# Kernel optimization log

Hardware: AMD Instinct MI355X
Metric: run time of the kernel (lower is better)

Reference implementation:

```python
import jax, jax.numpy as jnp
import numpy as np

B, N, F, H, L = 8, 512, 32, 64, 2

def setup_inputs() -> dict:
    key = jax.random.key(0)
    ks = jax.random.split(key, 16)
    s = lambda fan_in: 1.0 / np.sqrt(fan_in)
    return {
        "x": jax.random.normal(ks[0], (B, N, F), dtype=jnp.float32),
        # node encoder: Linear(F, H), stored as [in, out]
        "W_enc": jax.random.uniform(ks[1], (F, H), minval=-s(F), maxval=s(F)),
        "b_enc": jax.random.uniform(ks[2], (H,), minval=-s(F), maxval=s(F)),
        # edge MLP: Linear(2H, H) then Linear(H, 1)
        "W_e1": jax.random.uniform(ks[3], (2 * H, H), minval=-s(2 * H), maxval=s(2 * H)),
        "b_e1": jax.random.uniform(ks[4], (H,), minval=-s(2 * H), maxval=s(2 * H)),
        "W_e2": jax.random.uniform(ks[5], (H,), minval=-s(H), maxval=s(H)),
        "b_e2": jax.random.uniform(ks[6], (), minval=-s(H), maxval=s(H)),
        # per-layer message Linear(H, H)
        "W_msg": jax.random.uniform(ks[7], (L, H, H), minval=-s(H), maxval=s(H)),
        "b_msg": jax.random.uniform(ks[8], (L, H), minval=-s(H), maxval=s(H)),
        # per-layer GRUCell(H, H): gates ordered [r, z, n], stored as [in, 3H]
        "W_ih": jax.random.uniform(ks[9], (L, H, 3 * H), minval=-s(H), maxval=s(H)),
        "b_ih": jax.random.uniform(ks[10], (L, 3 * H), minval=-s(H), maxval=s(H)),
        "W_hh": jax.random.uniform(ks[11], (L, H, 3 * H), minval=-s(H), maxval=s(H)),
        "b_hh": jax.random.uniform(ks[12], (L, 3 * H), minval=-s(H), maxval=s(H)),
        # output Linear(H, 1)
        "W_out": jax.random.uniform(ks[13], (H, 1), minval=-s(H), maxval=s(H)),
        "b_out": jax.random.uniform(ks[14], (1,), minval=-s(H), maxval=s(H)),
    }

def reference(x, W_enc, b_enc, W_e1, b_e1, W_e2, b_e2, W_msg, b_msg,
              W_ih, b_ih, W_hh, b_hh, W_out, b_out):
    # Node encoding (dropout is eval-mode identity)
    h = jax.nn.relu(x @ W_enc + b_enc)  # [B, N, H]

    # Edge MLP on pairwise concat [h_i, h_j]: split W_e1 so we never build the 2H concat
    Wa, Wb = W_e1[:H], W_e1[H:]
    zi = h @ Wa                           # contribution of h_i, [B, N, H]
    zj = h @ Wb                           # contribution of h_j, [B, N, H]
    e = jax.nn.relu(zi[:, :, None, :] + zj[:, None, :, :] + b_e1)  # [B, N, N, H]
    logits = jnp.einsum('bijh,h->bij', e, W_e2) + b_e2             # [B, N, N]

    eye = jnp.eye(logits.shape[-1], dtype=bool)
    logits = jnp.where(eye[None], -jnp.inf, logits)
    adj = jax.nn.softmax(logits, axis=-1)
    adj = jnp.nan_to_num(adj, nan=0.0, posinf=0.0, neginf=0.0)

    for l in range(L):
        m = jnp.einsum('bij,bjh->bih', adj, h)             # message aggregation
        m = jax.nn.relu(m @ W_msg[l] + b_msg[l])
        # GRUCell update (gates [r, z, n])
        gi = m @ W_ih[l] + b_ih[l]
        gh = h @ W_hh[l] + b_hh[l]
        ir, iz, inn = jnp.split(gi, 3, axis=-1)
        hr, hz, hn = jnp.split(gh, 3, axis=-1)
        r = jax.nn.sigmoid(ir + hr)
        z = jax.nn.sigmoid(iz + hz)
        n = jnp.tanh(inn + r * hn)
        h = (1.0 - z) * n + z * h

    graph_emb = jnp.mean(h, axis=1)       # [B, H]
    return graph_emb @ W_out + b_out      # [B, 1]
```

## Files before the change

### kernel.cpp

```cpp
#include <hip/hip_runtime.h>
#include <math.h>

#define BB 8
#define NN 512
#define FF 32
#define HH 64
#define NEG_BIG (-1.0e30f)

__device__ __forceinline__ float lane_bcast(float v, int l) {
    return __int_as_float(__builtin_amdgcn_readlane(__float_as_int(v), l));
}

__global__ __launch_bounds__(256) void encode_kernel(
    const float* __restrict__ x, const float* __restrict__ W_enc,
    const float* __restrict__ b_enc, const float* __restrict__ W_e1,
    const float* __restrict__ b_e1,
    float* __restrict__ h, float* __restrict__ zi, float* __restrict__ zj)
{
    const int t = threadIdx.x;
    const int hh = t & 63;
    const int qu = __builtin_amdgcn_readfirstlane(t >> 6);
    const int gR = blockIdx.x * 4 + qu;

    const float xv = x[gR * FF + (hh & 31)];
    float acc = b_enc[hh];
#pragma unroll 8
    for (int k = 0; k < FF; ++k)
        acc = fmaf(lane_bcast(xv, k), W_enc[k * HH + hh], acc);
    const float hval = fmaxf(acc, 0.f);
    h[gR * HH + hh] = hval;

    float z1 = b_e1[hh], z2 = 0.f;
#pragma unroll 8
    for (int k = 0; k < HH; ++k) {
        const float hk = lane_bcast(hval, k);
        z1 = fmaf(hk, W_e1[k * HH + hh], z1);
        z2 = fmaf(hk, W_e1[(HH + k) * HH + hh], z2);
    }
    zi[gR * HH + hh] = z1;
    zj[gR * HH + hh] = z2;
}

template <int MODE>
__global__ __launch_bounds__(256, 2) void adjlayer_kernel(
    const float* __restrict__ zi, const float* __restrict__ zj,
    const float* __restrict__ We2, const float* __restrict__ be2,
    float* __restrict__ adjw, const float* __restrict__ h_in,
    const float* __restrict__ Wmsg, const float* __restrict__ bmsg,
    const float* __restrict__ Wih, const float* __restrict__ bih,
    const float* __restrict__ Whh, const float* __restrict__ bhh,
    float* __restrict__ h_out, float* __restrict__ partial)
{
    const int b  = blockIdx.x >> 6;
    const int i0 = (blockIdx.x & 63) << 3;
    const int t  = threadIdx.x;
    const int tj = t & 63;
    const int w  = __builtin_amdgcn_readfirstlane(t >> 6);
    const int gR0 = b * NN + i0;

    __shared__ float smem[NN * 17];
    __shared__ float mml[8][66];
    __shared__ float hol[8][66];
    __shared__ float redm[4][8];
    __shared__ float reds[4][8];

    float (*zjs)[17] = (float (*)[17])smem;
#define RED(p, r, c)       smem[(((p) * 8) + (r)) * 66 + (c)]
#define GP(h2, k2, r, g, c) smem[((((((h2) * 2 + (k2)) * 8) + (r)) * 3 + (g)) * 66) + (c)]

    const int r0 = 2 * w, r1 = 2 * w + 1;
    hol[r0][tj] = h_in[(size_t)(gR0 + r0) * HH + tj];
    hol[r1][tj] = h_in[(size_t)(gR0 + r1) * HH + tj];

    float va[8][2];
    if (MODE == 0) {
        float zir[8];
#pragma unroll
        for (int r = 0; r < 8; ++r) zir[r] = zi[(size_t)(gR0 + r) * HH + tj];
        const float wv = We2[tj];
        const float bias2 = be2[0];
        float acc[8][2];
#pragma unroll
        for (int r = 0; r < 8; ++r) { acc[r][0] = bias2; acc[r][1] = bias2; }

        for (int kp = 0; kp < 4; ++kp) {
            __syncthreads();
#pragma unroll
            for (int u = 0; u < 8; ++u) {
                const int i4 = t + u * 256;
                const int row = i4 >> 2, c4 = i4 & 3;
                *(float4*)&zjs[row][c4 * 4] =
                    ((const float4*)(zj + (size_t)(b * NN + row) * HH))[kp * 4 + c4];
            }
            __syncthreads();
            const int j0 = 128 * w + tj, j1 = j0 + 64;
#pragma unroll
            for (int kk = 0; kk < 16; ++kk) {
                const int k = (kp << 4) + kk;
                const float wk = lane_bcast(wv, k);
                const float zj0 = zjs[j0][kk];
                const float zj1 = zjs[j1][kk];
#pragma unroll
                for (int r = 0; r < 8; ++r) {
                    const float zv = lane_bcast(zir[r], k);
                    acc[r][0] = fmaf(fmaxf(zv + zj0, 0.f), wk, acc[r][0]);
                    acc[r][1] = fmaf(fmaxf(zv + zj1, 0.f), wk, acc[r][1]);
                }
            }
        }
#pragma unroll
        for (int r = 0; r < 8; ++r)
#pragma unroll
            for (int c = 0; c < 2; ++c)
                if (128 * w + 64 * c + tj == i0 + r) acc[r][c] = NEG_BIG;

#pragma unroll
        for (int r = 0; r < 8; ++r) {
            float m = fmaxf(acc[r][0], acc[r][1]);
#pragma unroll
            for (int off = 32; off >= 1; off >>= 1) m = fmaxf(m, __shfl_xor(m, off));
            if (tj == 0) redm[w][r] = m;
        }
        __syncthreads();
        float M[8];
#pragma unroll
        for (int r = 0; r < 8; ++r)
            M[r] = fmaxf(fmaxf(redm[0][r], redm[1][r]),
                         fmaxf(redm[2][r], redm[3][r]));
#pragma unroll
        for (int r = 0; r < 8; ++r) {
            const float e0 = __expf(acc[r][0] - M[r]);
            const float e1 = __expf(acc[r][1] - M[r]);
            va[r][0] = e0; va[r][1] = e1;
            float s = e0 + e1;
#pragma unroll
            for (int off = 32; off >= 1; off >>= 1) s += __shfl_xor(s, off);
            if (tj == 0) reds[w][r] = s;
        }
        __syncthreads();
#pragma unroll
        for (int r = 0; r < 8; ++r) {
            const float inv = 1.0f /
                (reds[0][r] + reds[1][r] + reds[2][r] + reds[3][r]);
            va[r][0] *= inv; va[r][1] *= inv;
            adjw[(size_t)(gR0 + r) * NN + 128 * w + tj]      = va[r][0];
            adjw[(size_t)(gR0 + r) * NN + 128 * w + 64 + tj] = va[r][1];
        }
    } else {
#pragma unroll
        for (int r = 0; r < 8; ++r) {
            va[r][0] = adjw[(size_t)(gR0 + r) * NN + 128 * w + tj];
            va[r][1] = adjw[(size_t)(gR0 + r) * NN + 128 * w + 64 + tj];
        }
    }

    {
        const float* hq = h_in + ((size_t)b * NN + 128 * w) * HH + tj;
        float mac[8] = {0.f, 0.f, 0.f, 0.f, 0.f, 0.f, 0.f, 0.f};
#pragma unroll
        for (int c = 0; c < 2; ++c) {
#pragma unroll 4
            for (int jj = 0; jj < 64; jj += 4) {
                const float h0 = hq[(64 * c + jj + 0) * HH];
                const float h1 = hq[(64 * c + jj + 1) * HH];
                const float h2 = hq[(64 * c + jj + 2) * HH];
                const float h3 = hq[(64 * c + jj + 3) * HH];
#pragma unroll
                for (int r = 0; r < 8; ++r) {
                    float a = fmaf(lane_bcast(va[r][c], jj + 0), h0, mac[r]);
                    a = fmaf(lane_bcast(va[r][c], jj + 1), h1, a);
                    a = fmaf(lane_bcast(va[r][c], jj + 2), h2, a);
                    mac[r] = fmaf(lane_bcast(va[r][c], jj + 3), h3, a);
                }
            }
        }
        if (MODE == 0) __syncthreads();
#pragma unroll
        for (int r = 0; r < 8; ++r) RED(w, r, tj) = mac[r];
    }
    __syncthreads();

    float mm0, mm1;
    {
        const float m0 = RED(0, r0, tj) + RED(1, r0, tj) + RED(2, r0, tj) + RED(3, r0, tj);
        const float m1 = RED(0, r1, tj) + RED(1, r1, tj) + RED(2, r1, tj) + RED(3, r1, tj);
        mm0 = bmsg[tj]; mm1 = mm0;
#pragma unroll 8
        for (int k = 0; k < HH; ++k) {
            const float wm = Wmsg[k * HH + tj];
            mm0 = fmaf(lane_bcast(m0, k), wm, mm0);
            mm1 = fmaf(lane_bcast(m1, k), wm, mm1);
        }
        mm0 = fmaxf(mm0, 0.f); mm1 = fmaxf(mm1, 0.f);
        mml[r0][tj] = mm0; mml[r1][tj] = mm1;
    }
    __syncthreads();

    {
        const int half = w >> 1, kh = w & 1;
        const float* Wg = half ? Whh : Wih;
        const float* bg = half ? bhh : bih;
        float sreg[8];
#pragma unroll
        for (int r = 0; r < 8; ++r) sreg[r] = half ? hol[r][tj] : mml[r][tj];
        float g0[8], g1[8], g2[8];
#pragma unroll
        for (int r = 0; r < 8; ++r) {
            g0[r] = kh ? 0.f : bg[tj];
            g1[r] = kh ? 0.f : bg[64 + tj];
            g2[r] = kh ? 0.f : bg[128 + tj];
        }
        const int k0 = kh * 32;
#pragma unroll 4
        for (int kk = 0; kk < 32; ++kk) {
            const float* wk = Wg + (size_t)(k0 + kk) * 192;
            const float w0 = wk[tj], w1 = wk[64 + tj], w2 = wk[128 + tj];
#pragma unroll
            for (int r = 0; r < 8; ++r) {
                const float s = lane_bcast(sreg[r], k0 + kk);
                g0[r] = fmaf(s, w0, g0[r]);
                g1[r] = fmaf(s, w1, g1[r]);
                g2[r] = fmaf(s, w2, g2[r]);
            }
        }
#pragma unroll
        for (int r = 0; r < 8; ++r) {
            GP(half, kh, r, 0, tj) = g0[r];
            GP(half, kh, r, 1, tj) = g1[r];
            GP(half, kh, r, 2, tj) = g2[r];
        }
    }
    __syncthreads();

    float hs0 = 0.f, hs1 = 0.f;
#pragma unroll
    for (int p = 0; p < 2; ++p) {
        const int rr = p ? r1 : r0;
        const float ir  = GP(0, 0, rr, 0, tj) + GP(0, 1, rr, 0, tj);
        const float iz  = GP(0, 0, rr, 1, tj) + GP(0, 1, rr, 1, tj);
        const float inn = GP(0, 0, rr, 2, tj) + GP(0, 1, rr, 2, tj);
        const float hr  = GP(1, 0, rr, 0, tj) + GP(1, 1, rr, 0, tj);
        const float hz  = GP(1, 0, rr, 1, tj) + GP(1, 1, rr, 1, tj);
        const float hn  = GP(1, 0, rr, 2, tj) + GP(1, 1, rr, 2, tj);
        const float rg = 1.f / (1.f + __expf(-(ir + hr)));
        const float zg = 1.f / (1.f + __expf(-(iz + hz)));
        const float ng = tanhf(inn + rg * hn);
        const float hnew = (1.f - zg) * ng + zg * hol[rr][tj];
        h_out[(size_t)(gR0 + rr) * HH + tj] = hnew;
        if (p) hs1 = hnew; else hs0 = hnew;
    }

    if (MODE == 1) {
        __syncthreads();
        mml[r0][tj] = hs0; mml[r1][tj] = hs1;
        __syncthreads();
        if (w == 0) {
            float s = 0.f;
#pragma unroll
            for (int r = 0; r < 8; ++r) s += mml[r][tj];
            partial[blockIdx.x * 64 + tj] = s;
        }
    }
#undef RED
#undef GP
}

__global__ __launch_bounds__(64) void readout_kernel(
    const float* __restrict__ partial, const float* __restrict__ W_out,
    const float* __restrict__ b_out, float* __restrict__ out)
{
    const int b = blockIdx.x;
    const int hh = threadIdx.x;
    float s = 0.f;
#pragma unroll 8
    for (int c = 0; c < 64; ++c)
        s += partial[(b * 64 + c) * 64 + hh];
    float v = s * (1.0f / NN) * W_out[hh];
#pragma unroll
    for (int off = 32; off >= 1; off >>= 1) v += __shfl_xor(v, off);
    if (hh == 0) out[b] = v + b_out[0];
}

extern "C" void kernel_launch(void* const* d_in, const int* in_sizes, int n_in,
                              void* d_out, int out_size, void* d_ws, size_t ws_size,
                              hipStream_t stream)
{
    const float* x     = (const float*)d_in[0];
    const float* W_enc = (const float*)d_in[1];
    const float* b_enc = (const float*)d_in[2];
    const float* W_e1  = (const float*)d_in[3];
    const float* b_e1  = (const float*)d_in[4];
    const float* W_e2  = (const float*)d_in[5];
    const float* b_e2  = (const float*)d_in[6];
    const float* W_msg = (const float*)d_in[7];
    const float* b_msg = (const float*)d_in[8];
    const float* W_ih  = (const float*)d_in[9];
    const float* b_ih  = (const float*)d_in[10];
    const float* W_hh  = (const float*)d_in[11];
    const float* b_hh  = (const float*)d_in[12];
    const float* W_out = (const float*)d_in[13];
    const float* b_out = (const float*)d_in[14];
    float* out = (float*)d_out;

    float* ws  = (float*)d_ws;
    float* h0  = ws;
    float* h1  = h0 + BB * NN * HH;
    float* zi  = h1 + BB * NN * HH;
    float* zj  = zi + BB * NN * HH;
    float* prt = zj + BB * NN * HH;
    float* adjw = prt + 512 * 64;

    encode_kernel<<<BB * NN / 4, 256, 0, stream>>>(x, W_enc, b_enc, W_e1, b_e1, h0, zi, zj);

    adjlayer_kernel<0><<<BB * (NN / 8), 256, 0, stream>>>(
        zi, zj, W_e2, b_e2, adjw, h0,
        W_msg, b_msg, W_ih, b_ih, W_hh, b_hh, h1, nullptr);
    adjlayer_kernel<1><<<BB * (NN / 8), 256, 0, stream>>>(
        zi, zj, W_e2, b_e2, adjw, h1,
        W_msg + HH * HH, b_msg + HH,
        W_ih + HH * 3 * HH, b_ih + 3 * HH, W_hh + HH * 3 * HH, b_hh + 3 * HH,
        h0, prt);

    readout_kernel<<<BB, 64, 0, stream>>>(prt, W_out, b_out, out);
}
```

Before: 82.92 us.

## Transpose zj in global memory and widen adjacency/layer kernel to 512 threads

The encoder now writes zj in a transposed [B, H, N] layout. Each thread of the adjacency kernel can then read its column j directly and coalesced from global memory, with no staging through shared memory. The kernel moves from 256 to 512 threads, so each thread handles one j column instead of two and the shared zj staging buffer is dropped. The softmax, message and GRU stages are re-split across 8 waves to match. The zi values and We2 weights are now read as uniform global loads instead of lane broadcasts. This trades shared-memory traffic and barriers for more global/scalar loads, with higher occupancy limits set via launch bounds.

```diff
diff --git a/kernel.cpp b/kernel.cpp
--- a/kernel.cpp
+++ b/kernel.cpp
@@ -15,7 +15,7 @@
     const float* __restrict__ x, const float* __restrict__ W_enc,
     const float* __restrict__ b_enc, const float* __restrict__ W_e1,
     const float* __restrict__ b_e1,
-    float* __restrict__ h, float* __restrict__ zi, float* __restrict__ zj)
+    float* __restrict__ h, float* __restrict__ zi, float* __restrict__ zjT)
 {
     const int t = threadIdx.x;
     const int hh = t & 63;
@@ -38,12 +38,12 @@
         z2 = fmaf(hk, W_e1[(HH + k) * HH + hh], z2);
     }
     zi[gR * HH + hh] = z1;
-    zj[gR * HH + hh] = z2;
+    zjT[((size_t)(gR >> 9) * HH + hh) * NN + (gR & (NN - 1))] = z2;
 }
 
 template <int MODE>
-__global__ __launch_bounds__(256, 2) void adjlayer_kernel(
-    const float* __restrict__ zi, const float* __restrict__ zj,
+__global__ __launch_bounds__(512, 4) void adjlayer_kernel(
+    const float* __restrict__ zi, const float* __restrict__ zjT,
     const float* __restrict__ We2, const float* __restrict__ be2,
     float* __restrict__ adjw, const float* __restrict__ h_in,
     const float* __restrict__ Wmsg, const float* __restrict__ bmsg,
@@ -57,66 +57,50 @@
     const int tj = t & 63;
     const int w  = __builtin_amdgcn_readfirstlane(t >> 6);
     const int gR0 = b * NN + i0;
-
-    __shared__ float smem[NN * 17];
+    const int j   = 64 * w + tj;
+
+    __shared__ float smem[6336];
     __shared__ float mml[8][66];
     __shared__ float hol[8][66];
-    __shared__ float redm[4][8];
-    __shared__ float reds[4][8];
-
-    float (*zjs)[17] = (float (*)[17])smem;
-#define RED(p, r, c)       smem[(((p) * 8) + (r)) * 66 + (c)]
-#define GP(h2, k2, r, g, c) smem[((((((h2) * 2 + (k2)) * 8) + (r)) * 3 + (g)) * 66) + (c)]
-
-    const int r0 = 2 * w, r1 = 2 * w + 1;
-    hol[r0][tj] = h_in[(size_t)(gR0 + r0) * HH + tj];
-    hol[r1][tj] = h_in[(size_t)(gR0 + r1) * HH + tj];
-
-    float va[8][2];
+    __shared__ float redm[8][8];
+    __shared__ float reds[8][8];
+#define RED(p, r, c)        smem[(((p) * 8) + (r)) * 66 + (c)]
+#define GP(h2, k2, r, g, c) smem[(((((h2) * 2 + (k2)) * 8 + (r)) * 3 + (g)) * 66) + (c)]
+
+    hol[w][tj] = h_in[(size_t)(gR0 + w) * HH + tj];
+
+    float va[8];
     if (MODE == 0) {
-        float zir[8];
-#pragma unroll
-        for (int r = 0; r < 8; ++r) zir[r] = zi[(size_t)(gR0 + r) * HH + tj];
-        const float wv = We2[tj];
+        const float* zib = zi + (size_t)gR0 * HH;
+        const float* ztb = zjT + (size_t)b * HH * NN + j;
         const float bias2 = be2[0];
-        float acc[8][2];
-#pragma unroll
-        for (int r = 0; r < 8; ++r) { acc[r][0] = bias2; acc[r][1] = bias2; }
-
-        for (int kp = 0; kp < 4; ++kp) {
-            __syncthreads();
-#pragma unroll
-            for (int u = 0; u < 8; ++u) {
-                const int i4 = t + u * 256;
-                const int row = i4 >> 2, c4 = i4 & 3;
-                *(float4*)&zjs[row][c4 * 4] =
-                    ((const float4*)(zj + (size_t)(b * NN + row) * HH))[kp * 4 + c4];
-            }
-            __syncthreads();
-            const int j0 = 128 * w + tj, j1 = j0 + 64;
-#pragma unroll
-            for (int kk = 0; kk < 16; ++kk) {
-                const int k = (kp << 4) + kk;
-                const float wk = lane_bcast(wv, k);
-                const float zj0 = zjs[j0][kk];
-                const float zj1 = zjs[j1][kk];
+        float acc[8];
+#pragma unroll
+        for (int r = 0; r < 8; ++r) acc[r] = bias2;
+
+        for (int kc = 0; kc < 8; ++kc) {
+            float zt[8];
+#pragma unroll
+            for (int kk = 0; kk < 8; ++kk)
+                zt[kk] = ztb[(size_t)(kc * 8 + kk) * NN];
+#pragma unroll
+            for (int kk = 0; kk < 8; ++kk) {
+                const int k = kc * 8 + kk;
+                const float wk = We2[k];
 #pragma unroll
                 for (int r = 0; r < 8; ++r) {
-                    const float zv = lane_bcast(zir[r], k);
-                    acc[r][0] = fmaf(fmaxf(zv + zj0, 0.f), wk, acc[r][0]);
-                    acc[r][1] = fmaf(fmaxf(zv + zj1, 0.f), wk, acc[r][1]);
+                    const float zv = zib[r * HH + k];
+                    acc[r] = fmaf(fmaxf(zv + zt[kk], 0.f), wk, acc[r]);
                 }
             }
         }
 #pragma unroll
         for (int r = 0; r < 8; ++r)
-#pragma unroll
-            for (int c = 0; c < 2; ++c)
-                if (128 * w + 64 * c + tj == i0 + r) acc[r][c] = NEG_BIG;
-
-#pragma unroll
-        for (int r = 0; r < 8; ++r) {
-            float m = fmaxf(acc[r][0], acc[r][1]);
+            if (j == i0 + r) acc[r] = NEG_BIG;
+
+#pragma unroll
+        for (int r = 0; r < 8; ++r) {
+            float m = acc[r];
 #pragma unroll
             for (int off = 32; off >= 1; off >>= 1) m = fmaxf(m, __shfl_xor(m, off));
             if (tj == 0) redm[w][r] = m;
@@ -124,15 +108,17 @@
         __syncthreads();
         float M[8];
 #pragma unroll
-        for (int r = 0; r < 8; ++r)
-            M[r] = fmaxf(fmaxf(redm[0][r], redm[1][r]),
-                         fmaxf(redm[2][r], redm[3][r]));
-#pragma unroll
-        for (int r = 0; r < 8; ++r) {
-            const float e0 = __expf(acc[r][0] - M[r]);
-            const float e1 = __expf(acc[r][1] - M[r]);
-            va[r][0] = e0; va[r][1] = e1;
-            float s = e0 + e1;
+        for (int r = 0; r < 8; ++r) {
+            float m = redm[0][r];
+#pragma unroll
+            for (int p = 1; p < 8; ++p) m = fmaxf(m, redm[p][r]);
+            M[r] = m;
+        }
+#pragma unroll
+        for (int r = 0; r < 8; ++r) {
+            const float e = __expf(acc[r] - M[r]);
+            va[r] = e;
+            float s = e;
 #pragma unroll
             for (int off = 32; off >= 1; off >>= 1) s += __shfl_xor(s, off);
             if (tj == 0) reds[w][r] = s;
@@ -140,72 +126,56 @@
         __syncthreads();
 #pragma unroll
         for (int r = 0; r < 8; ++r) {
-            const float inv = 1.0f /
-                (reds[0][r] + reds[1][r] + reds[2][r] + reds[3][r]);
-            va[r][0] *= inv; va[r][1] *= inv;
-            adjw[(size_t)(gR0 + r) * NN + 128 * w + tj]      = va[r][0];
-            adjw[(size_t)(gR0 + r) * NN + 128 * w + 64 + tj] = va[r][1];
+            float s = reds[0][r];
+#pragma unroll
+            for (int p = 1; p < 8; ++p) s += reds[p][r];
+            va[r] *= 1.0f / s;
+            adjw[(size_t)(gR0 + r) * NN + j] = va[r];
         }
     } else {
 #pragma unroll
-        for (int r = 0; r < 8; ++r) {
-            va[r][0] = adjw[(size_t)(gR0 + r) * NN + 128 * w + tj];
-            va[r][1] = adjw[(size_t)(gR0 + r) * NN + 128 * w + 64 + tj];
-        }
-    }
-
-    {
-        const float* hq = h_in + ((size_t)b * NN + 128 * w) * HH + tj;
+        for (int r = 0; r < 8; ++r)
+            va[r] = adjw[(size_t)(gR0 + r) * NN + j];
+    }
+
+    {
+        const float* hq = h_in + ((size_t)b * NN + 64 * w) * HH + tj;
         float mac[8] = {0.f, 0.f, 0.f, 0.f, 0.f, 0.f, 0.f, 0.f};
-#pragma unroll
-        for (int c = 0; c < 2; ++c) {
 #pragma unroll 4
-            for (int jj = 0; jj < 64; jj += 4) {
-                const float h0 = hq[(64 * c + jj + 0) * HH];
-                const float h1 = hq[(64 * c + jj + 1) * HH];
-                const float h2 = hq[(64 * c + jj + 2) * HH];
-                const float h3 = hq[(64 * c + jj + 3) * HH];
-#pragma unroll
-                for (int r = 0; r < 8; ++r) {
-                    float a = fmaf(lane_bcast(va[r][c], jj + 0), h0, mac[r]);
-                    a = fmaf(lane_bcast(va[r][c], jj + 1), h1, a);
-                    a = fmaf(lane_bcast(va[r][c], jj + 2), h2, a);
-                    mac[r] = fmaf(lane_bcast(va[r][c], jj + 3), h3, a);
-                }
-            }
-        }
-        if (MODE == 0) __syncthreads();
+        for (int jj = 0; jj < 64; ++jj) {
+            const float hv = hq[(size_t)jj * HH];
+#pragma unroll
+            for (int r = 0; r < 8; ++r)
+                mac[r] = fmaf(lane_bcast(va[r], jj), hv, mac[r]);
+        }
 #pragma unroll
         for (int r = 0; r < 8; ++r) RED(w, r, tj) = mac[r];
     }
     __syncthreads();
 
-    float mm0, mm1;
-    {
-        const float m0 = RED(0, r0, tj) + RED(1, r0, tj) + RED(2, r0, tj) + RED(3, r0, tj);
-        const float m1 = RED(0, r1, tj) + RED(1, r1, tj) + RED(2, r1, tj) + RED(3, r1, tj);
-        mm0 = bmsg[tj]; mm1 = mm0;
-#pragma unroll 8
-        for (int k = 0; k < HH; ++k) {
-            const float wm = Wmsg[k * HH + tj];
-            mm0 = fmaf(lane_bcast(m0, k), wm, mm0);
-            mm1 = fmaf(lane_bcast(m1, k), wm, mm1);
-        }
-        mm0 = fmaxf(mm0, 0.f); mm1 = fmaxf(mm1, 0.f);
-        mml[r0][tj] = mm0; mml[r1][tj] = mm1;
+    {
+        float m = RED(0, w, tj);
+#pragma unroll
+        for (int p = 1; p < 8; ++p) m += RED(p, w, tj);
+        float mmv = bmsg[tj];
+#pragma unroll 8
+        for (int k = 0; k < HH; ++k)
+            mmv = fmaf(lane_bcast(m, k), Wmsg[k * HH + tj], mmv);
+        mml[w][tj] = fmaxf(mmv, 0.f);
     }
     __syncthreads();
 
     {
-        const int half = w >> 1, kh = w & 1;
+        const int half = w >> 2, kh = (w >> 1) & 1, rq = w & 1;
         const float* Wg = half ? Whh : Wih;
         const float* bg = half ? bhh : bih;
-        float sreg[8];
-#pragma unroll
-        for (int r = 0; r < 8; ++r) sreg[r] = half ? hol[r][tj] : mml[r][tj];
-        float g0[8], g1[8], g2[8];
-#pragma unroll
-        for (int r = 0; r < 8; ++r) {
+        float sreg[4];
+#pragma unroll
+        for (int r = 0; r < 4; ++r)
+            sreg[r] = half ? hol[rq * 4 + r][tj] : mml[rq * 4 + r][tj];
+        float g0[4], g1[4], g2[4];
+#pragma unroll
+        for (int r = 0; r < 4; ++r) {
             g0[r] = kh ? 0.f : bg[tj];
             g1[r] = kh ? 0.f : bg[64 + tj];
             g2[r] = kh ? 0.f : bg[128 + tj];
@@ -216,7 +186,7 @@
             const float* wk = Wg + (size_t)(k0 + kk) * 192;
             const float w0 = wk[tj], w1 = wk[64 + tj], w2 = wk[128 + tj];
 #pragma unroll
-            for (int r = 0; r < 8; ++r) {
+            for (int r = 0; r < 4; ++r) {
                 const float s = lane_bcast(sreg[r], k0 + kk);
                 g0[r] = fmaf(s, w0, g0[r]);
                 g1[r] = fmaf(s, w1, g1[r]);
@@ -224,35 +194,32 @@
             }
         }
 #pragma unroll
-        for (int r = 0; r < 8; ++r) {
-            GP(half, kh, r, 0, tj) = g0[r];
-            GP(half, kh, r, 1, tj) = g1[r];
-            GP(half, kh, r, 2, tj) = g2[r];
+        for (int r = 0; r < 4; ++r) {
+            GP(half, kh, rq * 4 + r, 0, tj) = g0[r];
+            GP(half, kh, rq * 4 + r, 1, tj) = g1[r];
+            GP(half, kh, rq * 4 + r, 2, tj) = g2[r];
         }
     }
     __syncthreads();
 
-    float hs0 = 0.f, hs1 = 0.f;
-#pragma unroll
-    for (int p = 0; p < 2; ++p) {
-        const int rr = p ? r1 : r0;
-        const float ir  = GP(0, 0, rr, 0, tj) + GP(0, 1, rr, 0, tj);
-        const float iz  = GP(0, 0, rr, 1, tj) + GP(0, 1, rr, 1, tj);
-        const float inn = GP(0, 0, rr, 2, tj) + GP(0, 1, rr, 2, tj);
-        const float hr  = GP(1, 0, rr, 0, tj) + GP(1, 1, rr, 0, tj);
-        const float hz  = GP(1, 0, rr, 1, tj) + GP(1, 1, rr, 1, tj);
-        const float hn  = GP(1, 0, rr, 2, tj) + GP(1, 1, rr, 2, tj);
+    float hnew;
+    {
+        const float ir  = GP(0, 0, w, 0, tj) + GP(0, 1, w, 0, tj);
+        const float iz  = GP(0, 0, w, 1, tj) + GP(0, 1, w, 1, tj);
+        const float inn = GP(0, 0, w, 2, tj) + GP(0, 1, w, 2, tj);
+        const float hr  = GP(1, 0, w, 0, tj) + GP(1, 1, w, 0, tj);
+        const float hz  = GP(1, 0, w, 1, tj) + GP(1, 1, w, 1, tj);
+        const float hn  = GP(1, 0, w, 2, tj) + GP(1, 1, w, 2, tj);
         const float rg = 1.f / (1.f + __expf(-(ir + hr)));
         const float zg = 1.f / (1.f + __expf(-(iz + hz)));
         const float ng = tanhf(inn + rg * hn);
-        const float hnew = (1.f - zg) * ng + zg * hol[rr][tj];
-        h_out[(size_t)(gR0 + rr) * HH + tj] = hnew;
-        if (p) hs1 = hnew; else hs0 = hnew;
+        hnew = (1.f - zg) * ng + zg * hol[w][tj];
+        h_out[(size_t)(gR0 + w) * HH + tj] = hnew;
     }
 
     if (MODE == 1) {
         __syncthreads();
-        mml[r0][tj] = hs0; mml[r1][tj] = hs1;
+        mml[w][tj] = hnew;
         __syncthreads();
         if (w == 0) {
             float s = 0.f;
@@ -302,21 +269,21 @@
     const float* b_out = (const float*)d_in[14];
     float* out = (float*)d_out;
 
-    float* ws  = (float*)d_ws;
-    float* h0  = ws;
-    float* h1  = h0 + BB * NN * HH;
-    float* zi  = h1 + BB * NN * HH;
-    float* zj  = zi + BB * NN * HH;
-    float* prt = zj + BB * NN * HH;
+    float* ws   = (float*)d_ws;
+    float* h0   = ws;
+    float* h1   = h0 + BB * NN * HH;
+    float* zi   = h1 + BB * NN * HH;
+    float* zjT  = zi + BB * NN * HH;
+    float* prt  = zjT + BB * HH * NN;
     float* adjw = prt + 512 * 64;
 
-    encode_kernel<<<BB * NN / 4, 256, 0, stream>>>(x, W_enc, b_enc, W_e1, b_e1, h0, zi, zj);
-
-    adjlayer_kernel<0><<<BB * (NN / 8), 256, 0, stream>>>(
-        zi, zj, W_e2, b_e2, adjw, h0,
+    encode_kernel<<<BB * NN / 4, 256, 0, stream>>>(x, W_enc, b_enc, W_e1, b_e1, h0, zi, zjT);
+
+    adjlayer_kernel<0><<<BB * (NN / 8), 512, 0, stream>>>(
+        zi, zjT, W_e2, b_e2, adjw, h0,
         W_msg, b_msg, W_ih, b_ih, W_hh, b_hh, h1, nullptr);
-    adjlayer_kernel<1><<<BB * (NN / 8), 256, 0, stream>>>(
-        zi, zj, W_e2, b_e2, adjw, h1,
+    adjlayer_kernel<1><<<BB * (NN / 8), 512, 0, stream>>>(
+        zi, zjT, W_e2, b_e2, adjw, h1,
         W_msg + HH * HH, b_msg + HH,
         W_ih + HH * 3 * HH, b_ih + 3 * HH, W_hh + HH * 3 * HH, b_hh + 3 * HH,
         h0, prt);
```

Measured after the change: 73.25 us. 11.7% less time.
